# Optimization experiments

Measured on AMD Instinct MI355X. Metric: run time of the kernel, lower is better.

Reference implementation:

```python
import jax, jax.numpy as jnp
import numpy as np

B_, S_, IN_, D_, N_, K_ = 16, 4096, 64, 256, 16, 32


def _ln(x, g, b):
    m = jnp.mean(x, axis=-1, keepdims=True)
    v = jnp.var(x, axis=-1, keepdims=True)
    return (x - m) * jax.lax.rsqrt(v + 1e-5) * g + b


def setup_inputs() -> dict:
    key = jax.random.key(0)
    ks = jax.random.split(key, 24)
    s = 0.02
    d = dict(
        x=jax.random.normal(ks[0], (B_, S_, IN_), jnp.float32),
        W_in=jax.random.normal(ks[1], (IN_, D_)) * s, b_in=jnp.zeros((D_,)),
        ln1_g=jnp.ones((D_,)), ln1_b=jnp.zeros((D_,)),
        conv_w=jax.random.normal(ks[2], (D_, 1, 3)) * s, conv_b=jnp.zeros((D_,)),
        Wd=jax.random.normal(ks[3], (D_, D_)) * s, bd=jnp.zeros((D_,)),
        WB=jax.random.normal(ks[4], (D_, N_)) * s, bB=jnp.zeros((N_,)),
        WC=jax.random.normal(ks[5], (D_, N_)) * s, bC=jnp.zeros((N_,)),
        A=-jax.random.uniform(ks[6], (D_, N_)),
        Wg=jax.random.normal(ks[7], (D_, D_)) * s, bg=jnp.zeros((D_,)),
        filt_re=jax.random.normal(ks[8], (K_, D_)) * s,
        filt_im=jax.random.normal(ks[9], (K_, D_)) * s,
        alpha=jnp.ones((D_,)), beta=jnp.ones((D_,)),
        lnc_g=jnp.ones((D_,)), lnc_b=jnp.zeros((D_,)),
        W1=jax.random.normal(ks[10], (D_, D_ // 2)) * s, b1=jnp.zeros((D_ // 2,)),
        W2=jax.random.normal(ks[11], (D_ // 2, 2)) * s, b2=jnp.zeros((2,)),
    )
    return d


def reference(x, W_in, b_in, ln1_g, ln1_b, conv_w, conv_b, Wd, bd, WB, bB, WC, bC,
              A, Wg, bg, filt_re, filt_im, alpha, beta, lnc_g, lnc_b, W1, b1, W2, b2):
    xp = x @ W_in + b_in                                   # [B,S,D]

    # ---- TemporalBlock ----
    xn = _ln(xp, ln1_g, ln1_b)
    xc = jax.lax.conv_general_dilated(
        jnp.swapaxes(xn, 1, 2), conv_w, (1,), [(1, 1)],
        feature_group_count=D_, dimension_numbers=('NCH', 'OIH', 'NCH'))
    xc = jnp.swapaxes(xc + conv_b[:, None], 1, 2)          # [B,S,D]
    u = jax.nn.silu(xc)

    delta = jax.nn.softplus(u @ Wd + bd)                   # [B,S,D]
    Bm = u @ WB + bB                                       # [B,S,N]
    Cm = u @ WC + bC                                       # [B,S,N]

    def step(h, inp):
        u_t, d_t, B_t, C_t = inp                           # [B,D],[B,D],[B,N],[B,N]
        h = (1.0 + d_t[:, :, None] * A) * h + d_t[:, :, None] * B_t[:, None, :] * u_t[:, :, None]
        y_t = jnp.sum(C_t[:, None, :] * h, axis=-1)        # [B,D]
        return h, y_t

    h0 = jnp.zeros((u.shape[0], D_, N_), u.dtype)
    xs = tuple(jnp.swapaxes(a, 0, 1) for a in (u, delta, Bm, Cm))
    _, ys = jax.lax.scan(step, h0, xs)
    x_ssm = jnp.swapaxes(ys, 0, 1)                         # [B,S,D]
    g = jax.nn.silu(xn @ Wg + bg)
    x_t = xp + x_ssm * g

    # ---- SpectralBlock ----
    Xf = jnp.fft.rfft(xp, axis=1)                          # [B,F,D] complex
    mag = jnp.abs(Xf)
    _, idx = jax.lax.top_k(jnp.swapaxes(mag, 1, 2), K_)    # [B,D,K]
    idx = jnp.swapaxes(idx, 1, 2)                          # [B,K,D]
    sel = jnp.take_along_axis(Xf, idx, axis=1)             # [B,K,D]
    filt = filt_re + 1j * filt_im                          # [K,D]
    filtered = sel * filt[None]
    bi = jnp.arange(Xf.shape[0])[:, None, None]
    di = jnp.arange(D_)[None, None, :]
    Xfil = jnp.zeros_like(Xf).at[bi, idx, di].set(filtered)
    x_f = jnp.fft.irfft(Xfil, n=xp.shape[1], axis=1)       # [B,S,D]

    # ---- Fusion + classifier (eval: dropout = identity) ----
    z = alpha * x_t + beta * x_f
    zp = jnp.mean(z, axis=1)                               # [B,D]
    hcls = jax.nn.relu(_ln(zp, lnc_g, lnc_b) @ W1 + b1)
    return hcls @ W2 + b2                                  # [B,2]
```

## Files before the change

### kernel.cpp

```cpp
#include <hip/hip_runtime.h>
#include <hip/hip_bf16.h>
#include <math.h>

#define BB 16
#define SS 4096
#define IN 64
#define DD 256
#define NN 16
#define KK 32
#define CH 64
#define LCH 64
#define BS (BB*SS)

typedef __attribute__((ext_vector_type(4))) float f32x4;
typedef __attribute__((ext_vector_type(8))) short bf16x8;

__device__ __forceinline__ float bf2f(unsigned short u){
  return __uint_as_float(((unsigned int)u)<<16);
}
__device__ __forceinline__ unsigned short f2bf(float f){
  unsigned int u = __float_as_uint(f);
  return (unsigned short)((u + 0x7fffu + ((u>>16)&1u)) >> 16);
}
__device__ __forceinline__ float fast_softplus(float v){
  float e = __expf(-fabsf(v));
  return fmaxf(v, 0.f) + __logf(1.f + e);
}
__device__ __forceinline__ float fast_silu(float v){
  return v * __builtin_amdgcn_rcpf(1.f + __expf(-v));
}
__device__ __forceinline__ void* swz(void* base, int row, int byteoff){
  return (void*)((char*)base + (row<<9) + (byteoff ^ ((row&7)<<4)));
}
#define SW(i) ((i) ^ (((i)>>4)&15))

__global__ void k_prep(const float* Wd, const float* Wg, const float* WB, const float* WC,
                       const float* bBv, const float* bCv,
                       unsigned short* WdF, unsigned short* WgF,
                       float* bbc, float2* tw){
  int id = blockIdx.x*256 + threadIdx.x;
  if (id < 73728){
    int jn = id >> 12; int rem = id & 4095;
    int kc = rem >> 9; int l8 = (rem >> 3) & 63; int e = id & 7;
    int lr = l8 & 15, lh = l8 >> 4;
    int k = kc*32 + lh*8 + e;
    float v;
    if (jn < 16){ int n = jn*16 + lr; v = Wd[k*256+n]; }
    else { int c = (jn-16)*16 + lr; v = (c<16) ? WB[k*16+c] : WC[k*16+(c-16)]; }
    WdF[id] = f2bf(v);
  }
  else if (id < 139264){
    int o = id - 73728;
    int jn = o >> 12; int rem = o & 4095;
    int kc = rem >> 9; int l8 = (rem >> 3) & 63; int e = o & 7;
    int lr = l8 & 15, lh = l8 >> 4;
    int k = kc*32 + lh*8 + e;
    WgF[o] = f2bf(Wg[k*256 + jn*16 + lr]);
  }
  else if (id < 141312){ int k = id-139264;
    double a = -6.283185307179586476925287 * (double)k / 4096.0;
    tw[k] = make_float2((float)cos(a), (float)sin(a)); }
  else if (id < 141344){ int j = id-141312; bbc[j] = (j<16)? bBv[j] : bCv[j-16]; }
}

__global__ __launch_bounds__(256) void k_front(const float* x, const float* W_in, const float* b_in,
      const float* ln1_g, const float* ln1_b, const float* conv_w, const float* conv_b,
      float2* xpz, unsigned short* xn16, unsigned short* u16){
  __shared__ float xl[20][68];
  __shared__ float xs[20][260];
  __shared__ float lg[DD], lb[DD], c0w[DD], c1w[DD], c2w[DD], cbv[DD];
  int tid = threadIdx.x;
  int b = blockIdx.y; int t0 = blockIdx.x*16;
  lg[tid]=ln1_g[tid]; lb[tid]=ln1_b[tid];
  c0w[tid]=conv_w[tid*3]; c1w[tid]=conv_w[tid*3+1]; c2w[tid]=conv_w[tid*3+2];
  cbv[tid]=conv_b[tid];
  for (int i=tid; i<288; i+=256){
    int r = i>>4, kq = i&15;
    int t = t0 - 1 + r;
    float4 v = make_float4(0.f,0.f,0.f,0.f);
    if (t>=0 && t<SS) v = *(const float4*)&x[(size_t)((size_t)b*SS + t)*IN + kq*4];
    *(float4*)&xl[r][kq*4] = v;
  }
  __syncthreads();
  int ty = tid>>6, tx = tid&63;
  int c0 = tx*4;
  {
    float acc[5][4] = {};
    #pragma unroll 8
    for (int k=0;k<IN;k++){
      float4 wv = *(const float4*)&W_in[k*DD + c0];
      #pragma unroll
      for (int rr=0;rr<5;rr++){
        float xv = xl[ty+4*rr][k];
        acc[rr][0] = fmaf(xv, wv.x, acc[rr][0]);
        acc[rr][1] = fmaf(xv, wv.y, acc[rr][1]);
        acc[rr][2] = fmaf(xv, wv.z, acc[rr][2]);
        acc[rr][3] = fmaf(xv, wv.w, acc[rr][3]);
      }
    }
    float4 bv = *(const float4*)&b_in[c0];
    #pragma unroll
    for (int rr=0;rr<5;rr++){
      *(float4*)&xs[ty+4*rr][c0] = make_float4(acc[rr][0]+bv.x, acc[rr][1]+bv.y,
                                               acc[rr][2]+bv.z, acc[rr][3]+bv.w);
    }
  }
  __syncthreads();
  {
    int sl = tid&15, p0 = tid>>4;
    float2* dst = xpz + (size_t)b*128*SS + t0 + sl;
    #pragma unroll
    for (int pass=0; pass<8; pass++){
      int p = p0 + 16*pass;
      dst[(size_t)p*SS] = make_float2(xs[1+sl][2*p], xs[1+sl][2*p+1]);
    }
  }
  __syncthreads();
  int w = ty, lane = tx;
  for (int r=w; r<18; r+=4){
    int t = t0 - 1 + r;
    bool valid = (t>=0) && (t<SS);
    float4 v = *(const float4*)&xs[r][lane*4];
    float s1 = v.x+v.y+v.z+v.w;
    float s2 = v.x*v.x+v.y*v.y+v.z*v.z+v.w*v.w;
    #pragma unroll
    for (int off=32; off; off>>=1){ s1 += __shfl_xor(s1,off); s2 += __shfl_xor(s2,off); }
    float mean = s1*(1.f/256.f);
    float var  = s2*(1.f/256.f) - mean*mean;
    float rstd = rsqrtf(var + 1e-5f);
    float vv[4] = {v.x,v.y,v.z,v.w};
    float o[4];
    #pragma unroll
    for (int i=0;i<4;i++){
      int d = lane*4+i;
      o[i] = valid ? ((vv[i]-mean)*rstd*lg[d] + lb[d]) : 0.f;
    }
    *(float4*)&xs[r][lane*4] = make_float4(o[0],o[1],o[2],o[3]);
    if (r>=1 && r<=16){
      ushort4 st;
      st.x=f2bf(o[0]); st.y=f2bf(o[1]); st.z=f2bf(o[2]); st.w=f2bf(o[3]);
      *(ushort4*)&xn16[((size_t)b*SS + t)*DD + lane*4] = st;
    }
  }
  __syncthreads();
  int d = tid;
  float w0=c0w[d], w1=c1w[d], w2=c2w[d], cb=cbv[d];
  #pragma unroll 4
  for (int rr=0; rr<16; rr++){
    float a0=xs[rr][d], a1=xs[rr+1][d], a2=xs[rr+2][d];
    float xc = a0*w0 + a1*w1 + a2*w2 + cb;
    u16[((size_t)b*SS + (t0+rr))*DD + d] = f2bf(fast_silu(xc));
  }
}

template<int NTOT, int ACT>
__global__ __launch_bounds__(512,2) void k_gemm2(const unsigned short* Ab, const unsigned short* Bt,
      const float* bias_main, const float* bias_bc,
      unsigned short* out_main, unsigned short* out_bc){
  __shared__ unsigned short As[64*256];
  const int NF = NTOT/2;
  int tid = threadIdx.x;
  int m0 = blockIdx.x*64;
  {
    const uint4* gA = (const uint4*)(Ab + (size_t)m0*256);
    #pragma unroll
    for (int i=0;i<4;i++){
      int f = tid + 512*i;
      uint4 v = gA[f];
      *(uint4*)swz(As, f>>5, (f&31)<<4) = v;
    }
  }
  __syncthreads();
  int wv = tid>>6, lane = tid&63;
  int wm = wv>>1, nh = wv&1;
  int lr = lane&15, lh = lane>>4;
  const bf16x8* bbase = (const bf16x8*)(Bt + (size_t)(nh*NF)*4096 + (size_t)lane*8);
  f32x4 acc[NF];
  #pragma unroll
  for (int j=0;j<NF;j++){ acc[j][0]=0.f; acc[j][1]=0.f; acc[j][2]=0.f; acc[j][3]=0.f; }
  bf16x8 bq[2][8];
  #pragma unroll
  for (int kc=0;kc<8;kc++) bq[0][kc] = bbase[kc*64];
  #pragma unroll
  for (int j=0;j<NF;j++){
    if (j+1 < NF){
      #pragma unroll
      for (int kc=0;kc<8;kc++) bq[(j+1)&1][kc] = bbase[(j+1)*512 + kc*64];
    }
    #pragma unroll
    for (int kc=0;kc<8;kc++){
      bf16x8 af = *(const bf16x8*)swz(As, wm*16+lr, kc*64+lh*16);
      acc[j] = __builtin_amdgcn_mfma_f32_16x16x32_bf16(af, bq[j&1][kc], acc[j], 0,0,0);
    }
  }
  #pragma unroll
  for (int j=0;j<NF;j++){
    int jn = nh*NF + j;
    if (jn < 16){
      int col = jn*16 + lr;
      float bs = bias_main[col];
      #pragma unroll
      for (int i=0;i<4;i++){
        int row = m0 + wm*16 + lh*4 + i;
        float v = acc[j][i] + bs;
        if (ACT==1) v = fast_softplus(v);
        if (ACT==2) v = fast_silu(v);
        out_main[(size_t)row*256 + col] = f2bf(v);
      }
    } else {
      int col = (jn-16)*16 + lr;
      float bs = bias_bc[col];
      #pragma unroll
      for (int i=0;i<4;i++){
        int row = m0 + wm*16 + lh*4 + i;
        out_bc[(size_t)row*32 + col] = f2bf(acc[j][i] + bs);
      }
    }
  }
}

__global__ __launch_bounds__(256,2) void k_fft(const float2* xpz, const float2* twg, int* rank, float* T0){
  __shared__ float2 bufA[4096];
  __shared__ float2 bufB[4096];
  int blk = blockIdx.x;
  int b = blk >> 7, pair = blk & 127;
  int tid = threadIdx.x;
  const float4* src4 = (const float4*)(xpz + ((size_t)b*128 + pair)*SS);
  #pragma unroll
  for (int q=tid; q<2048; q+=256){
    float4 v = src4[q];
    bufA[SW(2*q)]   = make_float2(v.x, v.y);
    bufA[SW(2*q+1)] = make_float2(v.z, v.w);
  }
  __syncthreads();
  float2* s = bufA; float2* d = bufB;
  for (int st=0; st<6; st++){
    int m = 1<<(2*st);
    #pragma unroll
    for (int it=0; it<4; it++){
      int i = tid + 256*it;
      int k4 = i & (m-1);
      int tb = i - k4;
      float2 a0 = s[SW(i)];
      float2 a1 = s[SW(i+1024)];
      float2 a2 = s[SW(i+2048)];
      float2 a3 = s[SW(i+3072)];
      float2 w1 = twg[tb];
      float2 w2 = make_float2(fmaf(w1.x,w1.x,-w1.y*w1.y), 2.f*w1.x*w1.y);
      float2 w3 = make_float2(fmaf(w1.x,w2.x,-w1.y*w2.y), fmaf(w1.x,w2.y, w1.y*w2.x));
      float s0x=a0.x+a2.x, s0y=a0.y+a2.y;
      float s1x=a0.x-a2.x, s1y=a0.y-a2.y;
      float s2x=a1.x+a3.x, s2y=a1.y+a3.y;
      float t3x=a1.y-a3.y, t3y=a3.x-a1.x;
      int base = 4*i - 3*k4;
      d[SW(base)] = make_float2(s0x+s2x, s0y+s2y);
      float b1x = s1x+t3x, b1y = s1y+t3y;
      d[SW(base+m)]   = make_float2(fmaf(w1.x,b1x,-w1.y*b1y), fmaf(w1.x,b1y, w1.y*b1x));
      float b2x = s0x-s2x, b2y = s0y-s2y;
      d[SW(base+2*m)] = make_float2(fmaf(w2.x,b2x,-w2.y*b2y), fmaf(w2.x,b2y, w2.y*b2x));
      float b3x = s1x-t3x, b3y = s1y-t3y;
      d[SW(base+3*m)] = make_float2(fmaf(w3.x,b3x,-w3.y*b3y), fmaf(w3.x,b3y, w3.y*b3x));
    }
    __syncthreads();
    float2* t = s; s = d; d = t;
  }
  float2 z0 = s[0];
  float thx = 4.f*z0.x*z0.x, thy = 4.f*z0.y*z0.y;
  int cx=0, cy=0;
  #pragma unroll
  for (int j=0;j<8;j++){
    int f = 1 + tid + 256*j;
    float2 zf = s[SW(f)];
    float2 zc = s[SW(4096-f)];
    float sxr = zf.x+zc.x, sxi = zf.y-zc.y;
    float syr = zf.x-zc.x, syi = zf.y+zc.y;
    cx += (fmaf(sxr,sxr,sxi*sxi) > thx) ? 1 : 0;
    cy += (fmaf(syr,syr,syi*syi) > thy) ? 1 : 0;
  }
  #pragma unroll
  for (int off=32; off; off>>=1){ cx += __shfl_xor(cx, off); cy += __shfl_xor(cy, off); }
  int* scr = (int*)bufB;
  if ((tid&63)==0){ scr[tid>>6] = cx; scr[4+(tid>>6)] = cy; }
  __syncthreads();
  if (tid==0){
    int r0 = b*256 + 2*pair;
    rank[r0]   = scr[0]+scr[1]+scr[2]+scr[3];
    rank[r0+1] = scr[4]+scr[5]+scr[6]+scr[7];
    T0[r0]   = z0.x;
    T0[r0+1] = z0.y;
  }
}

__global__ __launch_bounds__(256) void k_scanA(const unsigned short* d16, const unsigned short* u16,
      const unsigned short* bc16, const float* Aw, float* AB_A, float* AB_B){
  __shared__ float bcs[LCH][32];
  int c = blockIdx.x, b = blockIdx.y;
  int t0 = c*LCH;
  int tid = threadIdx.x;
  {
    int t = tid>>2, q = tid&3;
    const unsigned short* src = bc16 + ((size_t)b*SS + t0 + t)*32 + q*8;
    uint4 v0 = *(const uint4*)src;
    const unsigned short* p0 = (const unsigned short*)&v0;
    float f[8];
    #pragma unroll
    for (int i=0;i<8;i++) f[i]=bf2f(p0[i]);
    *(float4*)&bcs[t][q*8]   = make_float4(f[0],f[1],f[2],f[3]);
    *(float4*)&bcs[t][q*8+4] = make_float4(f[4],f[5],f[6],f[7]);
  }
  __syncthreads();
  int d = tid;
  float aw[16];
  #pragma unroll
  for (int j=0;j<4;j++){
    float4 a4 = *(const float4*)&Aw[d*16 + j*4];
    aw[4*j]=a4.x; aw[4*j+1]=a4.y; aw[4*j+2]=a4.z; aw[4*j+3]=a4.w;
  }
  float Ac[16], Bc[16];
  #pragma unroll
  for (int n=0;n<16;n++){ Ac[n]=1.f; Bc[n]=0.f; }
  const unsigned short* dp = d16 + ((size_t)b*SS + t0)*DD + d;
  const unsigned short* up = u16 + ((size_t)b*SS + t0)*DD + d;
  #pragma unroll 8
  for (int t=0;t<LCH;t++){
    float de = bf2f(dp[(size_t)t*DD]);
    float uu = bf2f(up[(size_t)t*DD]);
    float du = de*uu;
    float4 b0 = *(const float4*)&bcs[t][0];
    float4 b1 = *(const float4*)&bcs[t][4];
    float4 b2 = *(const float4*)&bcs[t][8];
    float4 b3 = *(const float4*)&bcs[t][12];
    float bm[16] = {b0.x,b0.y,b0.z,b0.w, b1.x,b1.y,b1.z,b1.w,
                    b2.x,b2.y,b2.z,b2.w, b3.x,b3.y,b3.z,b3.w};
    #pragma unroll
    for (int n=0;n<16;n++){
      float a = fmaf(de, aw[n], 1.f);
      Ac[n] *= a;
      Bc[n] = fmaf(a, Bc[n], du*bm[n]);
    }
  }
  size_t o = (size_t)c*65536 + (size_t)b*4096 + (size_t)d*16;
  #pragma unroll
  for (int j=0;j<4;j++){
    *(float4*)&AB_A[o+4*j] = make_float4(Ac[4*j],Ac[4*j+1],Ac[4*j+2],Ac[4*j+3]);
    *(float4*)&AB_B[o+4*j] = make_float4(Bc[4*j],Bc[4*j+1],Bc[4*j+2],Bc[4*j+3]);
  }
}

__global__ void k_scanB(const float* AB_A, const float* AB_B, float* Hs){
  int tid = blockIdx.x*256 + threadIdx.x;
  float h = 0.f;
  #pragma unroll 8
  for (int c=0;c<CH;c++){
    Hs[c*65536 + tid] = h;
    h = fmaf(AB_A[c*65536 + tid], h, AB_B[c*65536 + tid]);
  }
}

__global__ __launch_bounds__(256) void k_scanC(const unsigned short* d16, const unsigned short* u16,
      const unsigned short* bc16, const unsigned short* g16, const float* Aw, const float* Hs, float* part){
  __shared__ float bcs[LCH][32];
  int c = blockIdx.x, b = blockIdx.y;
  int t0 = c*LCH;
  int tid = threadIdx.x;
  {
    int t = tid>>2, q = tid&3;
    const unsigned short* src = bc16 + ((size_t)b*SS + t0 + t)*32 + q*8;
    uint4 v0 = *(const uint4*)src;
    const unsigned short* p0 = (const unsigned short*)&v0;
    float f[8];
    #pragma unroll
    for (int i=0;i<8;i++) f[i]=bf2f(p0[i]);
    *(float4*)&bcs[t][q*8]   = make_float4(f[0],f[1],f[2],f[3]);
    *(float4*)&bcs[t][q*8+4] = make_float4(f[4],f[5],f[6],f[7]);
  }
  __syncthreads();
  int d = tid;
  float aw[16];
  #pragma unroll
  for (int j=0;j<4;j++){
    float4 a4 = *(const float4*)&Aw[d*16 + j*4];
    aw[4*j]=a4.x; aw[4*j+1]=a4.y; aw[4*j+2]=a4.z; aw[4*j+3]=a4.w;
  }
  float h[16];
  {
    size_t o = (size_t)c*65536 + (size_t)b*4096 + (size_t)d*16;
    #pragma unroll
    for (int j=0;j<4;j++){
      float4 h4 = *(const float4*)&Hs[o+4*j];
      h[4*j]=h4.x; h[4*j+1]=h4.y; h[4*j+2]=h4.z; h[4*j+3]=h4.w;
    }
  }
  float acc = 0.f;
  const unsigned short* dp = d16 + ((size_t)b*SS + t0)*DD + d;
  const unsigned short* up = u16 + ((size_t)b*SS + t0)*DD + d;
  const unsigned short* gp = g16 + ((size_t)b*SS + t0)*DD + d;
  #pragma unroll 8
  for (int t=0;t<LCH;t++){
    float de = bf2f(dp[(size_t)t*DD]);
    float uu = bf2f(up[(size_t)t*DD]);
    float gg = bf2f(gp[(size_t)t*DD]);
    float du = de*uu;
    float4 b0 = *(const float4*)&bcs[t][0];
    float4 b1 = *(const float4*)&bcs[t][4];
    float4 b2 = *(const float4*)&bcs[t][8];
    float4 b3 = *(const float4*)&bcs[t][12];
    float4 c0 = *(const float4*)&bcs[t][16];
    float4 c1 = *(const float4*)&bcs[t][20];
    float4 c2 = *(const float4*)&bcs[t][24];
    float4 c3 = *(const float4*)&bcs[t][28];
    float bm[16] = {b0.x,b0.y,b0.z,b0.w, b1.x,b1.y,b1.z,b1.w,
                    b2.x,b2.y,b2.z,b2.w, b3.x,b3.y,b3.z,b3.w};
    float cm[16] = {c0.x,c0.y,c0.z,c0.w, c1.x,c1.y,c1.z,c1.w,
                    c2.x,c2.y,c2.z,c2.w, c3.x,c3.y,c3.z,c3.w};
    float y0 = 0.f, y1 = 0.f;
    #pragma unroll
    for (int n=0;n<16;n+=2){
      float a0 = fmaf(de, aw[n],   1.f);
      float a1 = fmaf(de, aw[n+1], 1.f);
      h[n]   = fmaf(a0, h[n],   du*bm[n]);
      h[n+1] = fmaf(a1, h[n+1], du*bm[n+1]);
      y0 = fmaf(cm[n],   h[n],   y0);
      y1 = fmaf(cm[n+1], h[n+1], y1);
    }
    acc = fmaf(y0+y1, gg, acc);
  }
  part[(size_t)(b*256 + d)*CH + c] = acc;
}

__global__ __launch_bounds__(256) void k_final(const float* part, const float* T0, const int* rank,
      const float* alpha, const float* beta, const float* filt_re,
      const float* lnc_g, const float* lnc_b,
      const float* W1, const float* b1, const float* W2, const float* b2,
      float* out){
  __shared__ float zs[256];
  __shared__ float h1[128];
  __shared__ float red[8];
  int b = blockIdx.x, d = threadIdx.x;
  int row = b*256 + d;
  float ps = 0.f;
  #pragma unroll 8
  for (int c=0;c<CH;c++) ps += part[(size_t)row*CH + c];
  float ssm_mean = ps * (1.f/4096.f);
  float t0v = T0[row];
  float mxp = t0v * (1.f/4096.f);
  int r = rank[row];
  float spec = (r < KK) ? t0v * filt_re[r*DD + d] * (1.f/4096.f) : 0.f;
  float zp = alpha[d]*(mxp + ssm_mean) + beta[d]*spec;
  float s1 = zp, s2 = zp*zp;
  #pragma unroll
  for (int off=32; off; off>>=1){ s1 += __shfl_xor(s1,off); s2 += __shfl_xor(s2,off); }
  if ((d&63)==0){ red[d>>6] = s1; red[4+(d>>6)] = s2; }
  __syncthreads();
  float mean = (red[0]+red[1]+red[2]+red[3]) * (1.f/256.f);
  float var  = (red[4]+red[5]+red[6]+red[7]) * (1.f/256.f) - mean*mean;
  float ln = (zp-mean)*rsqrtf(var+1e-5f)*lnc_g[d] + lnc_b[d];
  zs[d] = ln;
  __syncthreads();
  if (d < 128){
    float acc = b1[d];
    #pragma unroll 16
    for (int k=0;k<256;k++) acc = fmaf(zs[k], W1[k*128+d], acc);
    h1[d] = fmaxf(acc, 0.f);
  }
  __syncthreads();
  if (d < 2){
    float acc = b2[d];
    #pragma unroll 16
    for (int k=0;k<128;k++) acc = fmaf(h1[k], W2[k*2+d], acc);
    out[b*2+d] = acc;
  }
}

extern "C" void kernel_launch(void* const* d_in, const int* in_sizes, int n_in,
                              void* d_out, int out_size, void* d_ws, size_t ws_size,
                              hipStream_t stream){
  const float* x      = (const float*)d_in[0];
  const float* W_in   = (const float*)d_in[1];
  const float* b_in   = (const float*)d_in[2];
  const float* ln1_g  = (const float*)d_in[3];
  const float* ln1_b  = (const float*)d_in[4];
  const float* conv_w = (const float*)d_in[5];
  const float* conv_b = (const float*)d_in[6];
  const float* Wd     = (const float*)d_in[7];
  const float* bd     = (const float*)d_in[8];
  const float* WB     = (const float*)d_in[9];
  const float* bB     = (const float*)d_in[10];
  const float* WC     = (const float*)d_in[11];
  const float* bC     = (const float*)d_in[12];
  const float* A      = (const float*)d_in[13];
  const float* Wg     = (const float*)d_in[14];
  const float* bg     = (const float*)d_in[15];
  const float* filt_re= (const float*)d_in[16];
  const float* alpha  = (const float*)d_in[18];
  const float* beta   = (const float*)d_in[19];
  const float* lnc_g  = (const float*)d_in[20];
  const float* lnc_b  = (const float*)d_in[21];
  const float* W1     = (const float*)d_in[22];
  const float* b1     = (const float*)d_in[23];
  const float* W2     = (const float*)d_in[24];
  const float* b2     = (const float*)d_in[25];

  char* w = (char*)d_ws;
  unsigned short* d16  = (unsigned short*)(w);
  unsigned short* bc16 = (unsigned short*)(w + 33554432);
  float2* xpz = (float2*)(w + 67108864);
  float* AB_A = (float*)(w + 67108864);
  float* AB_B = (float*)(w + 67108864 + 16777216);
  float* Hs   = (float*)(w + 67108864 + 33554432);
  float* part = (float*)(w + 67108864 + 50331648);
  unsigned short* xn16 = (unsigned short*)(w + 134217728);
  unsigned short* u16  = (unsigned short*)(w + 167772160);
  unsigned short* g16  = (unsigned short*)(w + 201326592);
  char* small = w + 234881024;
  unsigned short* WdF  = (unsigned short*)(small);
  unsigned short* WgF  = (unsigned short*)(small + 147456);
  float*  bbc = (float*)(small + 278528);
  float2* tw  = (float2*)(small + 278656);
  float*  T0  = (float*)(small + 295040);
  int*    rank= (int*)(small + 311424);
  (void)in_sizes; (void)n_in; (void)out_size; (void)ws_size;

  hipLaunchKernelGGL(k_prep, dim3(553), dim3(256), 0, stream,
                     Wd, Wg, WB, WC, bB, bC, WdF, WgF, bbc, tw);
  hipLaunchKernelGGL(k_front, dim3(SS/16, BB), dim3(256), 0, stream,
                     x, W_in, b_in, ln1_g, ln1_b, conv_w, conv_b, xpz, xn16, u16);
  hipLaunchKernelGGL(k_fft, dim3(BB*128), dim3(256), 0, stream, xpz, tw, rank, T0);
  hipLaunchKernelGGL((k_gemm2<18,1>), dim3(BS/64), dim3(512), 0, stream,
                     u16, WdF, bd, bbc, d16, bc16);
  hipLaunchKernelGGL((k_gemm2<16,2>), dim3(BS/64), dim3(512), 0, stream,
                     xn16, WgF, bg, bbc, g16, bc16);
  hipLaunchKernelGGL(k_scanA, dim3(CH, BB), dim3(256), 0, stream, d16, u16, bc16, A, AB_A, AB_B);
  hipLaunchKernelGGL(k_scanB, dim3(256), dim3(256), 0, stream, AB_A, AB_B, Hs);
  hipLaunchKernelGGL(k_scanC, dim3(CH, BB), dim3(256), 0, stream, d16, u16, bc16, g16, A, Hs, part);
  hipLaunchKernelGGL(k_final, dim3(BB), dim3(256), 0, stream,
                     part, T0, rank, alpha, beta, filt_re, lnc_g, lnc_b, W1, b1, W2, b2, (float*)d_out);
}
```

Measured before the change: 275.2 us.

## Make FFT kernel in-place with bit-reversed output to halve LDS and raise occupancy

```diff
diff --git a/kernel.cpp b/kernel.cpp
--- a/kernel.cpp
+++ b/kernel.cpp
@@ -33,6 +33,10 @@
   return (void*)((char*)base + (row<<9) + (byteoff ^ ((row&7)<<4)));
 }
 #define SW(i) ((i) ^ (((i)>>4)&15))
+__device__ __forceinline__ int rev4(int k){
+  return ((k&3)<<10) | (((k>>2)&3)<<8) | (((k>>4)&3)<<6)
+       | (((k>>6)&3)<<4) | (((k>>8)&3)<<2) | ((k>>10)&3);
+}
 
 __global__ void k_prep(const float* Wd, const float* Wg, const float* WB, const float* WC,
                        const float* bBv, const float* bCv,
@@ -112,7 +116,8 @@
     #pragma unroll
     for (int pass=0; pass<8; pass++){
       int p = p0 + 16*pass;
-      dst[(size_t)p*SS] = make_float2(xs[1+sl][2*p], xs[1+sl][2*p+1]);
+      float2 v = *(const float2*)&xs[1+sl][2*p];
+      dst[(size_t)p*SS] = v;
     }
   }
   __syncthreads();
@@ -219,9 +224,9 @@
   }
 }
 
-__global__ __launch_bounds__(256,2) void k_fft(const float2* xpz, const float2* twg, int* rank, float* T0){
-  __shared__ float2 bufA[4096];
-  __shared__ float2 bufB[4096];
+__global__ __launch_bounds__(256,4) void k_fft(const float2* xpz, const float2* twg, int* rank, float* T0){
+  __shared__ float2 buf[4096];
+  __shared__ int scr8[8];
   int blk = blockIdx.x;
   int b = blk >> 7, pair = blk & 127;
   int tid = threadIdx.x;
@@ -229,49 +234,47 @@
   #pragma unroll
   for (int q=tid; q<2048; q+=256){
     float4 v = src4[q];
-    bufA[SW(2*q)]   = make_float2(v.x, v.y);
-    bufA[SW(2*q+1)] = make_float2(v.z, v.w);
-  }
-  __syncthreads();
-  float2* s = bufA; float2* d = bufB;
+    buf[SW(2*q)]   = make_float2(v.x, v.y);
+    buf[SW(2*q+1)] = make_float2(v.z, v.w);
+  }
+  __syncthreads();
+  int m = 1024, fac = 1;
   for (int st=0; st<6; st++){
-    int m = 1<<(2*st);
     #pragma unroll
     for (int it=0; it<4; it++){
-      int i = tid + 256*it;
-      int k4 = i & (m-1);
-      int tb = i - k4;
-      float2 a0 = s[SW(i)];
-      float2 a1 = s[SW(i+1024)];
-      float2 a2 = s[SW(i+2048)];
-      float2 a3 = s[SW(i+3072)];
-      float2 w1 = twg[tb];
+      int t = tid + 256*it;
+      int j = t & (m-1);
+      int i0 = 4*t - 3*j;
+      float2 a0 = buf[SW(i0)];
+      float2 a1 = buf[SW(i0+m)];
+      float2 a2 = buf[SW(i0+2*m)];
+      float2 a3 = buf[SW(i0+3*m)];
+      float2 w1 = twg[j*fac];
       float2 w2 = make_float2(fmaf(w1.x,w1.x,-w1.y*w1.y), 2.f*w1.x*w1.y);
       float2 w3 = make_float2(fmaf(w1.x,w2.x,-w1.y*w2.y), fmaf(w1.x,w2.y, w1.y*w2.x));
-      float s0x=a0.x+a2.x, s0y=a0.y+a2.y;
-      float s1x=a0.x-a2.x, s1y=a0.y-a2.y;
-      float s2x=a1.x+a3.x, s2y=a1.y+a3.y;
+      float t0x=a0.x+a2.x, t0y=a0.y+a2.y;
+      float t1x=a0.x-a2.x, t1y=a0.y-a2.y;
+      float t2x=a1.x+a3.x, t2y=a1.y+a3.y;
       float t3x=a1.y-a3.y, t3y=a3.x-a1.x;
-      int base = 4*i - 3*k4;
-      d[SW(base)] = make_float2(s0x+s2x, s0y+s2y);
-      float b1x = s1x+t3x, b1y = s1y+t3y;
-      d[SW(base+m)]   = make_float2(fmaf(w1.x,b1x,-w1.y*b1y), fmaf(w1.x,b1y, w1.y*b1x));
-      float b2x = s0x-s2x, b2y = s0y-s2y;
-      d[SW(base+2*m)] = make_float2(fmaf(w2.x,b2x,-w2.y*b2y), fmaf(w2.x,b2y, w2.y*b2x));
-      float b3x = s1x-t3x, b3y = s1y-t3y;
-      d[SW(base+3*m)] = make_float2(fmaf(w3.x,b3x,-w3.y*b3y), fmaf(w3.x,b3y, w3.y*b3x));
+      buf[SW(i0)]     = make_float2(t0x+t2x, t0y+t2y);
+      float b1x = t1x+t3x, b1y = t1y+t3y;
+      buf[SW(i0+m)]   = make_float2(fmaf(w1.x,b1x,-w1.y*b1y), fmaf(w1.x,b1y, w1.y*b1x));
+      float b2x = t0x-t2x, b2y = t0y-t2y;
+      buf[SW(i0+2*m)] = make_float2(fmaf(w2.x,b2x,-w2.y*b2y), fmaf(w2.x,b2y, w2.y*b2x));
+      float b3x = t1x-t3x, b3y = t1y-t3y;
+      buf[SW(i0+3*m)] = make_float2(fmaf(w3.x,b3x,-w3.y*b3y), fmaf(w3.x,b3y, w3.y*b3x));
     }
     __syncthreads();
-    float2* t = s; s = d; d = t;
-  }
-  float2 z0 = s[0];
+    m >>= 2; fac <<= 2;
+  }
+  float2 z0 = buf[0];
   float thx = 4.f*z0.x*z0.x, thy = 4.f*z0.y*z0.y;
   int cx=0, cy=0;
   #pragma unroll
   for (int j=0;j<8;j++){
     int f = 1 + tid + 256*j;
-    float2 zf = s[SW(f)];
-    float2 zc = s[SW(4096-f)];
+    float2 zf = buf[SW(rev4(f))];
+    float2 zc = buf[SW(rev4(4096-f))];
     float sxr = zf.x+zc.x, sxi = zf.y-zc.y;
     float syr = zf.x-zc.x, syi = zf.y+zc.y;
     cx += (fmaf(sxr,sxr,sxi*sxi) > thx) ? 1 : 0;
@@ -279,13 +282,12 @@
   }
   #pragma unroll
   for (int off=32; off; off>>=1){ cx += __shfl_xor(cx, off); cy += __shfl_xor(cy, off); }
-  int* scr = (int*)bufB;
-  if ((tid&63)==0){ scr[tid>>6] = cx; scr[4+(tid>>6)] = cy; }
+  if ((tid&63)==0){ scr8[tid>>6] = cx; scr8[4+(tid>>6)] = cy; }
   __syncthreads();
   if (tid==0){
     int r0 = b*256 + 2*pair;
-    rank[r0]   = scr[0]+scr[1]+scr[2]+scr[3];
-    rank[r0+1] = scr[4]+scr[5]+scr[6]+scr[7];
+    rank[r0]   = scr8[0]+scr8[1]+scr8[2]+scr8[3];
+    rank[r0+1] = scr8[4]+scr8[5]+scr8[6]+scr8[7];
     T0[r0]   = z0.x;
     T0[r0+1] = z0.y;
   }
```

New measurement: 273.6 us. About the same (-0.6%).
